# Kernel optimization log

Hardware: AMD Instinct MI355X
Metric: run time of the kernel (lower is better)

## Reference

```python
import jax, jax.numpy as jnp
import numpy as np

N_NODES, IN_DIM, HID, N_CLS, N_T = 4096, 512, 256, 128, 20


def _odefunc(x, A, Wt, bt):
    # X' = relu(Linear(A @ X)); dropout=0.0 so it is the identity
    return jax.nn.relu((A @ x) @ Wt.T + bt)


def _rk4_traj(vt, x0, A, Wt, bt):
    # torchdiffeq 'rk4' = fixed-grid 3/8-rule RK4 stepping between consecutive vt points
    f = lambda y: _odefunc(y, A, Wt, bt)  # autonomous: t unused by ODEFunc

    def step(x, dt):
        k1 = f(x)
        k2 = f(x + dt * k1 / 3.0)
        k3 = f(x + dt * (k2 - k1 / 3.0))
        k4 = f(x + dt * (k1 - k2 + k3))
        xn = x + dt * (k1 + 3.0 * k2 + 3.0 * k3 + k4) / 8.0
        return xn, xn

    dts = vt[1:] - vt[:-1]
    _, ys = jax.lax.scan(step, x0, dts)
    return jnp.concatenate([x0[None], ys], axis=0)  # [T, N, H]


def setup_inputs() -> dict:
    key = jax.random.key(0)
    ks = jax.random.split(key, 8)
    vt = jnp.arange(N_T, dtype=jnp.float32) * 0.05  # increasing time ticks, horizon ~1.0
    x = jax.random.normal(ks[0], (N_NODES, IN_DIM), dtype=jnp.float32)
    # row-scaled dense adjacency (torch.mm dense path); spectral scale ~O(1)
    A = jax.random.uniform(ks[1], (N_NODES, N_NODES), dtype=jnp.float32) / N_NODES
    W1 = jax.random.normal(ks[2], (HID, IN_DIM), dtype=jnp.float32) / np.sqrt(IN_DIM)
    b1 = jnp.zeros((HID,), dtype=jnp.float32)
    W2 = jax.random.normal(ks[3], (HID, HID), dtype=jnp.float32) / np.sqrt(HID)
    b2 = jnp.zeros((HID,), dtype=jnp.float32)
    Wt = jax.random.normal(ks[4], (HID, HID), dtype=jnp.float32) * (0.5 / np.sqrt(HID))
    bt = jnp.zeros((HID,), dtype=jnp.float32)
    Wo = jax.random.normal(ks[5], (N_CLS, HID), dtype=jnp.float32) / np.sqrt(HID)
    bo = jnp.zeros((N_CLS,), dtype=jnp.float32)
    return {"vt": vt, "x": x, "A": A, "W1": W1, "b1": b1, "W2": W2,
            "b2": b2, "Wt": Wt, "bt": bt, "Wo": Wo, "bo": bo}


def reference(vt, x, A, W1, b1, W2, b2, Wt, bt, Wo, bo):
    # input_layer: Linear -> Tanh -> Linear (dropout = 0.0 elsewhere)
    h = jnp.tanh(x @ W1.T + b1) @ W2.T + b2            # [N, H]
    traj = _rk4_traj(vt, h, A, Wt, bt)                 # [T, N, H] (terminal=False -> full trajectory)
    return traj @ Wo.T + bo                            # [T, N, C]
```

## Files before the change

### kernel.cpp

```cpp
#include <hip/hip_runtime.h>
#include <stdint.h>

typedef __bf16 bf16;
typedef bf16 bf16x8 __attribute__((ext_vector_type(8)));
typedef float f32x4 __attribute__((ext_vector_type(4)));
typedef uint32_t u32;
typedef unsigned long long u64;
typedef unsigned char u8;

#define NN   4096
#define HID  256
#define NCLS 128

__device__ __forceinline__ void gload16(const void* g, void* l) {
  __builtin_amdgcn_global_load_lds((const __attribute__((address_space(1))) u32*)g,
                                   (__attribute__((address_space(3))) u32*)l, 16, 0, 0);
}

__global__ void convf2b(const float* __restrict__ s, bf16* __restrict__ d, int n) {
  int i = (blockIdx.x * blockDim.x + threadIdx.x) * 4;
  if (i >= n) return;
  f32x4 v = *(const f32x4*)(s + i);
  bf16 o[4] = {(bf16)v[0], (bf16)v[1], (bf16)v[2], (bf16)v[3]};
  *(u64*)(d + i) = *(u64*)o;
}

__global__ void convAf8(const float* __restrict__ s, u8* __restrict__ d, int n) {
  int i = (blockIdx.x * blockDim.x + threadIdx.x) * 4;
  if (i >= n) return;
  f32x4 v = *(const f32x4*)(s + i);
  u32 pk = __builtin_amdgcn_cvt_pk_fp8_f32(v[0] * 4096.f, v[1] * 4096.f, 0, false);
  pk = __builtin_amdgcn_cvt_pk_fp8_f32(v[2] * 4096.f, v[3] * 4096.f, pk, true);
  *(u32*)(d + i) = pk;
}

__device__ __forceinline__ f32x4 ksplit_reduce(char* smem, f32x4 acc[2][2],
                                               int kw, int sw, int hh, int rl) {
  float* fs = (float*)smem;
  #pragma unroll
  for (int q = 0; q < 4; ++q) {
    const int src = (kw < q) ? kw : kw - 1;
    float* dst = fs + ((q * 3 + src) * 2 + sw) * 272;
    const int mf = q >> 1, nf = q & 1;
    if (q != kw) {
      #pragma unroll
      for (int j = 0; j < 4; ++j) dst[(hh * 4 + j) * 17 + rl] = acc[mf][nf][j];
    }
  }
  asm volatile("s_waitcnt lgkmcnt(0)" ::: "memory");
  __builtin_amdgcn_s_barrier();
  f32x4 r;
  if (kw == 0)      r = acc[0][0];
  else if (kw == 1) r = acc[0][1];
  else if (kw == 2) r = acc[1][0];
  else              r = acc[1][1];
  #pragma unroll
  for (int src = 0; src < 3; ++src) {
    const float* sp = fs + ((kw * 3 + src) * 2 + sw) * 272;
    #pragma unroll
    for (int j = 0; j < 4; ++j) r[j] += sp[(hh * 4 + j) * 17 + rl];
  }
  return r;
}

__global__ __launch_bounds__(512, 2) void gemmf8(
    const u8* __restrict__ Ag,
    const u8* __restrict__ Bg,
    bf16* __restrict__ Cb)
{
  __shared__ __align__(16) char smem[73728];
  const int tid = threadIdx.x;
  const int l = tid & 63, wv = tid >> 6;
  const int kw = wv & 3, sw = wv >> 2;
  const int rl = l & 15, hh = l >> 4;

  const int chunk = gridDim.x >> 3;
  const int sb = (blockIdx.x & 7) * chunk + (blockIdx.x >> 3);
  const int m0 = (sb >> 3) * 64, n0 = (sb & 7) * 32;

  const bool isB = wv >= 4;
  const int w4 = wv & 3;
  const int rlo = l >> 3, gq = l & 7;
  const int sg = gq ^ rlo;
  const int grow = (isB ? n0 + w4 * 8 : m0 + w4 * 16) + rlo;
  const u8* sG = (isB ? Bg : Ag) + (size_t)grow * 4096 + sg * 16;
  const int stoff = isB ? 8192 + w4 * 1024 : w4 * 2048;

  f32x4 acc[2][2];
  #pragma unroll
  for (int i = 0; i < 2; ++i)
    #pragma unroll
    for (int j = 0; j < 2; ++j) acc[i][j] = (f32x4){0.f, 0.f, 0.f, 0.f};

  auto stage = [&](int buf, int t) {
    char* base = smem + buf * 12288 + stoff;
    const u8* g = sG + t * 128;
    gload16(g, base);
    if (!isB) gload16(g + 8 * 4096, base + 1024);
  };

  const int g0 = kw * 2 + (hh >> 1);
  const int co = ((g0 ^ (rl & 7)) << 4) + (hh & 1) * 8;
  auto compute = [&](int buf) {
    const char* As = smem + buf * 12288;
    const char* Bs = As + 8192;
    u64 a0 = *(const u64*)(As + (sw * 32 + rl +  0) * 128 + co);
    u64 a1 = *(const u64*)(As + (sw * 32 + rl + 16) * 128 + co);
    u64 b0 = *(const u64*)(Bs + (rl +  0) * 128 + co);
    u64 b1 = *(const u64*)(Bs + (rl + 16) * 128 + co);
    __builtin_amdgcn_s_setprio(1);
    acc[0][0] = __builtin_amdgcn_mfma_f32_16x16x32_fp8_fp8((long)a0, (long)b0, acc[0][0], 0, 0, 0);
    acc[0][1] = __builtin_amdgcn_mfma_f32_16x16x32_fp8_fp8((long)a0, (long)b1, acc[0][1], 0, 0, 0);
    acc[1][0] = __builtin_amdgcn_mfma_f32_16x16x32_fp8_fp8((long)a1, (long)b0, acc[1][0], 0, 0, 0);
    acc[1][1] = __builtin_amdgcn_mfma_f32_16x16x32_fp8_fp8((long)a1, (long)b1, acc[1][1], 0, 0, 0);
    __builtin_amdgcn_s_setprio(0);
  };

  stage(0, 0); stage(1, 1); stage(2, 2); stage(3, 3); stage(4, 4);
  int cur = 0, pre = 5;
  for (int t = 0; t < 32; ++t) {
    const int rem = 31 - t;
    const int fut = rem < 4 ? rem : 4;
    if (!isB) {
      if (fut == 4)      { asm volatile("s_waitcnt vmcnt(8)" ::: "memory"); }
      else if (fut == 3) { asm volatile("s_waitcnt vmcnt(6)" ::: "memory"); }
      else if (fut == 2) { asm volatile("s_waitcnt vmcnt(4)" ::: "memory"); }
      else if (fut == 1) { asm volatile("s_waitcnt vmcnt(2)" ::: "memory"); }
      else               { asm volatile("s_waitcnt vmcnt(0)" ::: "memory"); }
    } else {
      if (fut == 4)      { asm volatile("s_waitcnt vmcnt(4)" ::: "memory"); }
      else if (fut == 3) { asm volatile("s_waitcnt vmcnt(3)" ::: "memory"); }
      else if (fut == 2) { asm volatile("s_waitcnt vmcnt(2)" ::: "memory"); }
      else if (fut == 1) { asm volatile("s_waitcnt vmcnt(1)" ::: "memory"); }
      else               { asm volatile("s_waitcnt vmcnt(0)" ::: "memory"); }
    }
    __builtin_amdgcn_sched_barrier(0);
    __builtin_amdgcn_s_barrier();
    __builtin_amdgcn_sched_barrier(0);
    if (t + 5 < 32) stage(pre, t + 5);
    compute(cur);
    cur = (cur == 5) ? 0 : cur + 1;
    pre = (pre == 5) ? 0 : pre + 1;
  }
  __builtin_amdgcn_s_barrier();
  __builtin_amdgcn_sched_barrier(0);

  f32x4 o = ksplit_reduce(smem, acc, kw, sw, hh, rl);
  const int row0 = m0 + sw * 32 + (kw >> 1) * 16 + hh * 4;
  const int col  = n0 + (kw & 1) * 16 + rl;
  #pragma unroll
  for (int r = 0; r < 4; ++r)
    Cb[(row0 + r) * HID + col] = (bf16)(o[r] * 2.44140625e-4f);
}

template<int EPI, int KK>
__global__ __launch_bounds__(512, 2) void gemmbf(
    const bf16* __restrict__ Ag, int lda,
    const bf16* __restrict__ Bg, int ldb,
    int Ntiles,
    const float* __restrict__ bias,
    float* __restrict__ outf,
    bf16* __restrict__ outb,
    u8* __restrict__ ybt,
    float* __restrict__ xbuf,
    const float* __restrict__ kk1,
    const float* __restrict__ kk2,
    const float* __restrict__ kk3,
    const float* __restrict__ vt, int step)
{
  __shared__ __align__(16) char smem[49152];
  const int tid = threadIdx.x;
  const int l = tid & 63, wv = tid >> 6;
  const int kw = wv & 3, sw = wv >> 2;
  const int rl = l & 15, hh = l >> 4;

  const int chunk = gridDim.x >> 3;
  const int sb = (blockIdx.x & 7) * chunk + (blockIdx.x >> 3);
  const int mtile = sb / Ntiles;
  const int ntile = sb - mtile * Ntiles;
  const int m0 = mtile * 64, n0 = ntile * 32;

  const bool isB = wv >= 4;
  const int w4 = wv & 3;

  f32x4 acc[2][2];
  #pragma unroll
  for (int i = 0; i < 2; ++i)
    #pragma unroll
    for (int j = 0; j < 2; ++j) acc[i][j] = (f32x4){0.f, 0.f, 0.f, 0.f};

  if constexpr (KK == 256) {
    const int lrow = l >> 5, lg = l & 31;
    if (!isB) {
      const char* gb = (const char*)(Ag + (size_t)(m0 + w4 * 16) * lda);
      char* base = smem + w4 * 8192;
      #pragma unroll
      for (int i = 0; i < 8; ++i) {
        const int r = i * 2 + lrow;
        const int swz = (lg ^ ((w4 * 16 + r) & 7)) << 4;
        gload16(gb + (size_t)r * lda * 2 + swz, base + i * 1024);
      }
    } else {
      const char* gb = (const char*)(Bg + (size_t)(n0 + w4 * 8) * ldb);
      char* base = smem + 32768 + w4 * 4096;
      #pragma unroll
      for (int i = 0; i < 4; ++i) {
        const int r = i * 2 + lrow;
        const int swz = (lg ^ ((w4 * 8 + r) & 7)) << 4;
        gload16(gb + (size_t)r * ldb * 2 + swz, base + i * 1024);
      }
    }
    asm volatile("s_waitcnt vmcnt(0)" ::: "memory");
    __builtin_amdgcn_sched_barrier(0);
    __builtin_amdgcn_s_barrier();
    __builtin_amdgcn_sched_barrier(0);

    const char* As = smem;
    const char* Bs = smem + 32768;
    #pragma unroll
    for (int ks = 0; ks < 2; ++ks) {
      const int ca = ((((kw * 2 + ks) * 4 + hh) ^ (rl & 7)) << 4);
      bf16x8 a0 = *(const bf16x8*)(As + (sw * 32 + rl +  0) * 512 + ca);
      bf16x8 a1 = *(const bf16x8*)(As + (sw * 32 + rl + 16) * 512 + ca);
      bf16x8 b0 = *(const bf16x8*)(Bs + (rl +  0) * 512 + ca);
      bf16x8 b1 = *(const bf16x8*)(Bs + (rl + 16) * 512 + ca);
      __builtin_amdgcn_s_setprio(1);
      acc[0][0] = __builtin_amdgcn_mfma_f32_16x16x32_bf16(a0, b0, acc[0][0], 0, 0, 0);
      acc[0][1] = __builtin_amdgcn_mfma_f32_16x16x32_bf16(a0, b1, acc[0][1], 0, 0, 0);
      acc[1][0] = __builtin_amdgcn_mfma_f32_16x16x32_bf16(a1, b0, acc[1][0], 0, 0, 0);
      acc[1][1] = __builtin_amdgcn_mfma_f32_16x16x32_bf16(a1, b1, acc[1][1], 0, 0, 0);
      __builtin_amdgcn_s_setprio(0);
    }
    __builtin_amdgcn_s_barrier();
    __builtin_amdgcn_sched_barrier(0);
  } else {
    const int rlo = l >> 4, gq = l & 15;
    const size_t ldby = (size_t)(isB ? ldb : lda) * 2;
    const int grow = (isB ? n0 + w4 * 8 : m0 + w4 * 16) + rlo;
    const char* sGb = (const char*)(isB ? (const void*)Bg : (const void*)Ag)
                      + (size_t)grow * ldby;
    const int c0 = (gq ^ rlo) << 4;
    const int c1 = (gq ^ (rlo + 4)) << 4;
    const int stoff = isB ? 16384 + w4 * 2048 : w4 * 4096;

    auto stage = [&](int buf, int t) {
      char* base = smem + buf * 24576 + stoff;
      const char* g = sGb + (size_t)t * 256;
      gload16(g + c0,            base);
      gload16(g + 4 * ldby + c1, base + 1024);
      if (!isB) {
        gload16(g +  8 * ldby + c0, base + 2048);
        gload16(g + 12 * ldby + c1, base + 3072);
      }
    };

    const int ca = ((kw * 4 + hh) ^ (rl & 7)) << 4;
    auto compute = [&](int buf) {
      const char* As = smem + buf * 24576;
      const char* Bs = As + 16384;
      bf16x8 a0 = *(const bf16x8*)(As + (sw * 32 + rl +  0) * 256 + ca);
      bf16x8 a1 = *(const bf16x8*)(As + (sw * 32 + rl + 16) * 256 + ca);
      bf16x8 b0 = *(const bf16x8*)(Bs + (rl +  0) * 256 + ca);
      bf16x8 b1 = *(const bf16x8*)(Bs + (rl + 16) * 256 + ca);
      __builtin_amdgcn_s_setprio(1);
      acc[0][0] = __builtin_amdgcn_mfma_f32_16x16x32_bf16(a0, b0, acc[0][0], 0, 0, 0);
      acc[0][1] = __builtin_amdgcn_mfma_f32_16x16x32_bf16(a0, b1, acc[0][1], 0, 0, 0);
      acc[1][0] = __builtin_amdgcn_mfma_f32_16x16x32_bf16(a1, b0, acc[1][0], 0, 0, 0);
      acc[1][1] = __builtin_amdgcn_mfma_f32_16x16x32_bf16(a1, b1, acc[1][1], 0, 0, 0);
      __builtin_amdgcn_s_setprio(0);
    };

    const int nmac = KK >> 7;
    stage(0, 0);
    asm volatile("s_waitcnt vmcnt(0)" ::: "memory");
    __builtin_amdgcn_s_barrier();
    int cur = 0;
    for (int t = 0; t < nmac; ++t) {
      if (t + 1 < nmac) stage(cur ^ 1, t + 1);
      compute(cur);
      asm volatile("s_waitcnt vmcnt(0)" ::: "memory");
      __builtin_amdgcn_sched_barrier(0);
      __builtin_amdgcn_s_barrier();
      cur ^= 1;
    }
    __builtin_amdgcn_sched_barrier(0);
  }

  f32x4 o = ksplit_reduce(smem, acc, kw, sw, hh, rl);
  const int row0 = m0 + sw * 32 + (kw >> 1) * 16 + hh * 4;
  const int col  = n0 + (kw & 1) * 16 + rl;

  float dtv = 0.f;
  if constexpr (EPI >= 3 && EPI <= 6) dtv = vt[step + 1] - vt[step];

  if constexpr (EPI == 1) {
    #pragma unroll
    for (int r = 0; r < 4; ++r)
      outb[(row0 + r) * HID + col] = (bf16)tanhf(o[r] + bias[col]);
  } else if constexpr (EPI == 2) {
    float yv[4];
    #pragma unroll
    for (int r = 0; r < 4; ++r) {
      float v = o[r] + bias[col];
      xbuf[(row0 + r) * HID + col] = v;
      outb[(row0 + r) * HID + col] = (bf16)v;
      yv[r] = v;
    }
    u32 pk = __builtin_amdgcn_cvt_pk_fp8_f32(yv[0], yv[1], 0, false);
    pk = __builtin_amdgcn_cvt_pk_fp8_f32(yv[2], yv[3], pk, true);
    *(u32*)(ybt + (size_t)col * NN + row0) = pk;
  } else if constexpr (EPI >= 3 && EPI <= 6) {
    float yv[4];
    #pragma unroll
    for (int r = 0; r < 4; ++r) {
      const int idx = (row0 + r) * HID + col;
      float v = fmaxf(o[r] + bias[col], 0.f);
      float xv = xbuf[idx];
      float y;
      if constexpr (EPI == 3)      { outf[idx] = v; y = xv + dtv * (1.f/3.f) * v; }
      else if constexpr (EPI == 4) { outf[idx] = v; y = xv + dtv * (v - kk1[idx] * (1.f/3.f)); }
      else if constexpr (EPI == 5) { outf[idx] = v; y = xv + dtv * (kk1[idx] - kk2[idx] + v); }
      else {
        float xn = xv + dtv * 0.125f * (kk1[idx] + 3.f*kk2[idx] + 3.f*kk3[idx] + v);
        xbuf[idx] = xn;
        outb[idx] = (bf16)xn;
        y = xn;
      }
      yv[r] = y;
    }
    u32 pk = __builtin_amdgcn_cvt_pk_fp8_f32(yv[0], yv[1], 0, false);
    pk = __builtin_amdgcn_cvt_pk_fp8_f32(yv[2], yv[3], pk, true);
    *(u32*)(ybt + (size_t)col * NN + row0) = pk;
  } else {
    #pragma unroll
    for (int r = 0; r < 4; ++r)
      outf[(size_t)(row0 + r) * NCLS + col] = o[r] + bias[col];
  }
}

extern "C" void kernel_launch(void* const* d_in, const int* in_sizes, int n_in,
                              void* d_out, int out_size, void* d_ws, size_t ws_size,
                              hipStream_t stream)
{
  const float* vt = (const float*)d_in[0];
  const float* x  = (const float*)d_in[1];
  const float* A  = (const float*)d_in[2];
  const float* W1 = (const float*)d_in[3];
  const float* b1 = (const float*)d_in[4];
  const float* W2 = (const float*)d_in[5];
  const float* b2 = (const float*)d_in[6];
  const float* Wt = (const float*)d_in[7];
  const float* bt = (const float*)d_in[8];
  const float* Wo = (const float*)d_in[9];
  const float* bo = (const float*)d_in[10];
  float* out = (float*)d_out;

  char* p = (char*)d_ws;
  auto carve = [&](size_t n) { char* r = p; p += (n + 255) & ~(size_t)255; return r; };
  u8*   A8  = (u8*)carve((size_t)4096 * 4096);
  bf16* xb  = (bf16*)carve((size_t)4096 * 512 * 2);
  bf16* W1b = (bf16*)carve((size_t)256 * 512 * 2);
  bf16* W2b = (bf16*)carve((size_t)256 * 256 * 2);
  bf16* Wtb = (bf16*)carve((size_t)256 * 256 * 2);
  bf16* Wob = (bf16*)carve((size_t)128 * 256 * 2);
  bf16* T1b = (bf16*)carve((size_t)4096 * 256 * 2);
  bf16* Cb  = (bf16*)carve((size_t)4096 * 256 * 2);
  u8*   Y8  = (u8*)carve((size_t)256 * 4096);
  float* xs = (float*)carve((size_t)4096 * 256 * 4);
  float* k1 = (float*)carve((size_t)4096 * 256 * 4);
  float* k2 = (float*)carve((size_t)4096 * 256 * 4);
  float* k3 = (float*)carve((size_t)4096 * 256 * 4);
  size_t base_need = (size_t)(p - (char*)d_ws);
  const size_t trajBytes = (size_t)20 * 4096 * 256 * 2;
  bool big = (ws_size >= base_need + trajBytes);
  bf16* traj = (bf16*)carve(big ? trajBytes : (size_t)4096 * 256 * 2);

  convAf8<<<16384, 256, 0, stream>>>(A,  A8,  16777216);
  convf2b<<<2048,  256, 0, stream>>>(x,  xb,  2097152);
  convf2b<<<128,   256, 0, stream>>>(W1, W1b, 131072);
  convf2b<<<64,    256, 0, stream>>>(W2, W2b, 65536);
  convf2b<<<64,    256, 0, stream>>>(Wt, Wtb, 65536);
  convf2b<<<32,    256, 0, stream>>>(Wo, Wob, 32768);

  gemmbf<1, 512><<<512, 512, 0, stream>>>(xb, 512, W1b, 512, 8, b1,
      nullptr, T1b, nullptr, nullptr, nullptr, nullptr, nullptr, vt, 0);
  gemmbf<2, 256><<<512, 512, 0, stream>>>(T1b, 256, W2b, 256, 8, b2,
      nullptr, traj, Y8, xs, nullptr, nullptr, nullptr, vt, 0);
  if (!big)
    gemmbf<7, 256><<<256, 512, 0, stream>>>(traj, 256, Wob, 256, 4, bo,
        out, nullptr, nullptr, nullptr, nullptr, nullptr, nullptr, vt, 0);

  for (int t = 0; t < 19; ++t) {
    bf16* slot = big ? (traj + (size_t)(t + 1) * 4096 * 256) : traj;
    gemmf8<<<512, 512, 0, stream>>>(A8, Y8, Cb);
    gemmbf<3, 256><<<512, 512, 0, stream>>>(Cb, 256, Wtb, 256, 8, bt,
        k1, nullptr, Y8, xs, nullptr, nullptr, nullptr, vt, t);
    gemmf8<<<512, 512, 0, stream>>>(A8, Y8, Cb);
    gemmbf<4, 256><<<512, 512, 0, stream>>>(Cb, 256, Wtb, 256, 8, bt,
        k2, nullptr, Y8, xs, k1, nullptr, nullptr, vt, t);
    gemmf8<<<512, 512, 0, stream>>>(A8, Y8, Cb);
    gemmbf<5, 256><<<512, 512, 0, stream>>>(Cb, 256, Wtb, 256, 8, bt,
        k3, nullptr, Y8, xs, k1, k2, nullptr, vt, t);
    gemmf8<<<512, 512, 0, stream>>>(A8, Y8, Cb);
    gemmbf<6, 256><<<512, 512, 0, stream>>>(Cb, 256, Wtb, 256, 8, bt,
        nullptr, slot, Y8, xs, k1, k2, k3, vt, t);
    if (!big)
      gemmbf<7, 256><<<256, 512, 0, stream>>>(traj, 256, Wob, 256, 4, bo,
          out + (size_t)(t + 1) * 4096 * 128, nullptr, nullptr, nullptr,
          nullptr, nullptr, nullptr, vt, 0);
  }
  if (big)
    gemmbf<7, 256><<<5120, 512, 0, stream>>>(traj, 256, Wob, 256, 4, bo,
        out, nullptr, nullptr, nullptr, nullptr, nullptr, nullptr, vt, 0);
}
```

Before: 1.681 ms.

## Double K-tile width in fp8 GEMM and shrink pipeline to three stages

The fp8 A@X GEMM now stages 256-byte K tiles instead of 128-byte ones, so there are 16 main-loop iterations instead of 32. Each iteration issues two MFMA groups per wave, and the ring buffer drops from six stages to three, each twice as large. The aim is to halve the barrier and waitcnt overhead per unit of K work while keeping shared memory at the same 72 KB. The cost is a shallower prefetch depth, which may expose more global-load latency.

Result: faster. 1.434 ms, median of 2 (-14.7%).

```diff
diff --git a/kernel.cpp b/kernel.cpp
--- a/kernel.cpp
+++ b/kernel.cpp
@@ -80,11 +80,13 @@
 
   const bool isB = wv >= 4;
   const int w4 = wv & 3;
-  const int rlo = l >> 3, gq = l & 7;
-  const int sg = gq ^ rlo;
-  const int grow = (isB ? n0 + w4 * 8 : m0 + w4 * 16) + rlo;
-  const u8* sG = (isB ? Bg : Ag) + (size_t)grow * 4096 + sg * 16;
-  const int stoff = isB ? 8192 + w4 * 1024 : w4 * 2048;
+  const int rlo = l >> 4;
+  const int gq = l & 15;
+  const int rowbase = isB ? n0 + w4 * 8 : m0 + w4 * 16;
+  const u8* sGbase = (isB ? Bg : Ag) + (size_t)rowbase * 4096;
+  const int c0 = (gq ^ rlo) << 4;
+  const int c1 = (gq ^ (rlo + 4)) << 4;
+  const int stoff = isB ? 16384 + w4 * 2048 : w4 * 4096;
 
   f32x4 acc[2][2];
   #pragma unroll
@@ -93,54 +95,50 @@
     for (int j = 0; j < 2; ++j) acc[i][j] = (f32x4){0.f, 0.f, 0.f, 0.f};
 
   auto stage = [&](int buf, int t) {
-    char* base = smem + buf * 12288 + stoff;
-    const u8* g = sG + t * 128;
-    gload16(g, base);
-    if (!isB) gload16(g + 8 * 4096, base + 1024);
+    char* base = smem + buf * 24576 + stoff;
+    const u8* g = sGbase + (size_t)rlo * 4096 + t * 256;
+    gload16(g + c0,                      base);
+    gload16(g + (size_t)4  * 4096 + c1,  base + 1024);
+    if (!isB) {
+      gload16(g + (size_t)8  * 4096 + c0, base + 2048);
+      gload16(g + (size_t)12 * 4096 + c1, base + 3072);
+    }
   };
 
-  const int g0 = kw * 2 + (hh >> 1);
-  const int co = ((g0 ^ (rl & 7)) << 4) + (hh & 1) * 8;
   auto compute = [&](int buf) {
-    const char* As = smem + buf * 12288;
-    const char* Bs = As + 8192;
-    u64 a0 = *(const u64*)(As + (sw * 32 + rl +  0) * 128 + co);
-    u64 a1 = *(const u64*)(As + (sw * 32 + rl + 16) * 128 + co);
-    u64 b0 = *(const u64*)(Bs + (rl +  0) * 128 + co);
-    u64 b1 = *(const u64*)(Bs + (rl + 16) * 128 + co);
-    __builtin_amdgcn_s_setprio(1);
-    acc[0][0] = __builtin_amdgcn_mfma_f32_16x16x32_fp8_fp8((long)a0, (long)b0, acc[0][0], 0, 0, 0);
-    acc[0][1] = __builtin_amdgcn_mfma_f32_16x16x32_fp8_fp8((long)a0, (long)b1, acc[0][1], 0, 0, 0);
-    acc[1][0] = __builtin_amdgcn_mfma_f32_16x16x32_fp8_fp8((long)a1, (long)b0, acc[1][0], 0, 0, 0);
-    acc[1][1] = __builtin_amdgcn_mfma_f32_16x16x32_fp8_fp8((long)a1, (long)b1, acc[1][1], 0, 0, 0);
-    __builtin_amdgcn_s_setprio(0);
+    const char* As = smem + buf * 24576;
+    const char* Bs = As + 16384;
+    #pragma unroll
+    for (int ks = 0; ks < 2; ++ks) {
+      const int g0 = (kw * 2 + ks) * 2 + (hh >> 1);
+      const int co = ((g0 ^ (rl & 7)) << 4) + (hh & 1) * 8;
+      u64 a0 = *(const u64*)(As + (sw * 32 + rl +  0) * 256 + co);
+      u64 a1 = *(const u64*)(As + (sw * 32 + rl + 16) * 256 + co);
+      u64 b0 = *(const u64*)(Bs + (rl +  0) * 256 + co);
+      u64 b1 = *(const u64*)(Bs + (rl + 16) * 256 + co);
+      __builtin_amdgcn_s_setprio(1);
+      acc[0][0] = __builtin_amdgcn_mfma_f32_16x16x32_fp8_fp8((long)a0, (long)b0, acc[0][0], 0, 0, 0);
+      acc[0][1] = __builtin_amdgcn_mfma_f32_16x16x32_fp8_fp8((long)a0, (long)b1, acc[0][1], 0, 0, 0);
+      acc[1][0] = __builtin_amdgcn_mfma_f32_16x16x32_fp8_fp8((long)a1, (long)b0, acc[1][0], 0, 0, 0);
+      acc[1][1] = __builtin_amdgcn_mfma_f32_16x16x32_fp8_fp8((long)a1, (long)b1, acc[1][1], 0, 0, 0);
+      __builtin_amdgcn_s_setprio(0);
+    }
   };
 
-  stage(0, 0); stage(1, 1); stage(2, 2); stage(3, 3); stage(4, 4);
-  int cur = 0, pre = 5;
-  for (int t = 0; t < 32; ++t) {
-    const int rem = 31 - t;
-    const int fut = rem < 4 ? rem : 4;
-    if (!isB) {
-      if (fut == 4)      { asm volatile("s_waitcnt vmcnt(8)" ::: "memory"); }
-      else if (fut == 3) { asm volatile("s_waitcnt vmcnt(6)" ::: "memory"); }
-      else if (fut == 2) { asm volatile("s_waitcnt vmcnt(4)" ::: "memory"); }
-      else if (fut == 1) { asm volatile("s_waitcnt vmcnt(2)" ::: "memory"); }
-      else               { asm volatile("s_waitcnt vmcnt(0)" ::: "memory"); }
-    } else {
-      if (fut == 4)      { asm volatile("s_waitcnt vmcnt(4)" ::: "memory"); }
-      else if (fut == 3) { asm volatile("s_waitcnt vmcnt(3)" ::: "memory"); }
-      else if (fut == 2) { asm volatile("s_waitcnt vmcnt(2)" ::: "memory"); }
-      else if (fut == 1) { asm volatile("s_waitcnt vmcnt(1)" ::: "memory"); }
-      else               { asm volatile("s_waitcnt vmcnt(0)" ::: "memory"); }
-    }
+  stage(0, 0); stage(1, 1);
+  int cur = 0, pre = 2;
+  for (int t = 0; t < 16; ++t) {
+    if (t < 15) {
+      if (!isB) { asm volatile("s_waitcnt vmcnt(4)" ::: "memory"); }
+      else      { asm volatile("s_waitcnt vmcnt(2)" ::: "memory"); }
+    } else       { asm volatile("s_waitcnt vmcnt(0)" ::: "memory"); }
     __builtin_amdgcn_sched_barrier(0);
     __builtin_amdgcn_s_barrier();
     __builtin_amdgcn_sched_barrier(0);
-    if (t + 5 < 32) stage(pre, t + 5);
+    if (t + 2 < 16) stage(pre, t + 2);
     compute(cur);
-    cur = (cur == 5) ? 0 : cur + 1;
-    pre = (pre == 5) ? 0 : pre + 1;
+    cur = (cur == 2) ? 0 : cur + 1;
+    pre = (pre == 2) ? 0 : pre + 1;
   }
   __builtin_amdgcn_s_barrier();
   __builtin_amdgcn_sched_barrier(0);
```
